# Performance work log

Hardware: AMD Instinct MI355X
Metric: run time of the kernel (lower is better)

Reference implementation:

```python
import jax, jax.numpy as jnp
import numpy as np

N_NODES = 100000
N_EDGES = 3200000
IN_CH = 256


def setup_inputs() -> dict:
    key = jax.random.key(0)
    k1, k2, k3 = jax.random.split(key, 3)
    x = jax.random.normal(k1, (N_NODES, IN_CH), dtype=jnp.float32)
    edge_index = jax.random.randint(k2, (2, N_EDGES), 0, N_NODES, dtype=jnp.int64)
    # GCNConv linear: weight [in_channels, 1] (applied as x @ W), bias [1]
    W = jax.random.normal(k3, (IN_CH, 1), dtype=jnp.float32) * (1.0 / np.sqrt(IN_CH))
    b = jnp.zeros((1,), dtype=jnp.float32)
    return {"x": x, "edge_index": edge_index, "W": W, "b": b}


def reference(x, edge_index, W, b):
    # PyG GCNConv(in, 1): h = x @ W; add self-loops; symmetric norm; scatter-add to target; + bias
    N = x.shape[0]
    self_loops = jnp.broadcast_to(jnp.arange(N, dtype=edge_index.dtype)[None, :], (2, N))
    ei = jnp.concatenate([edge_index, self_loops], axis=1)  # [2, E+N]
    src, dst = ei[0], ei[1]

    # degree computed at target (col) with unit edge weights, incl. self-loops
    deg = jax.ops.segment_sum(jnp.ones(ei.shape[1], dtype=x.dtype), dst, num_segments=N)
    deg_inv_sqrt = jnp.where(deg > 0, jax.lax.rsqrt(deg), 0.0)
    norm = deg_inv_sqrt[src] * deg_inv_sqrt[dst]  # [E+N]

    h = x @ W  # [N, 1] — project first (out_channels < in_channels)
    msg = norm[:, None] * h[src]  # [E+N, 1]
    out = jax.ops.segment_sum(msg, dst, num_segments=N)  # [N, 1]
    return out + b
```

## Files before the change

kernel.cpp:

```cpp
#include <hip/hip_runtime.h>

#define GCN_N 100000
#define GCN_E 3200000
#define GCN_C 256
#define BSHIFT 8
#define NBUCK 391
#define BCAP 9216

#define NBLK 512
#define TB 1024
#define CHUNK (GCN_E / NBLK)
#define EPT ((CHUNK + TB - 1) / TB)
#define ROWS ((GCN_N + NBLK - 1) / NBLK)

__global__ void k_init(int* __restrict__ cursor) {
    const int i = threadIdx.x;
    if (i < NBUCK) cursor[i] = 0;
}

__global__ void __launch_bounds__(TB) k_proj_bin(const float* __restrict__ x,
                                                 const float* __restrict__ W,
                                                 float* __restrict__ h,
                                                 const int* __restrict__ src,
                                                 const int* __restrict__ dst,
                                                 int* __restrict__ cursor,
                                                 int* __restrict__ bpack) {
    __shared__ int hist[NBUCK];
    __shared__ int lscan[NBUCK];
    __shared__ int gbase[NBUCK];
    __shared__ int wsum[16], woff[16];
    __shared__ int spack[CHUNK];
    __shared__ int sdest[CHUNK];
    const int tid = threadIdx.x, blk = blockIdx.x;
    const int lane = tid & 63, wv = tid >> 6;

    for (int b = tid; b < NBUCK; b += TB) hist[b] = 0;
    __syncthreads();

    const int c0 = blk * CHUNK;
    int my_pack[EPT], my_b[EPT], my_off[EPT];
    #pragma unroll
    for (int j = 0; j < EPT; ++j) {
        const int k = tid + j * TB;
        my_b[j] = -1;
        if (k < CHUNK) {
            const int d = dst[c0 + k];
            const int s = src[c0 + k];
            const int b = d >> BSHIFT;
            my_pack[j] = (s << BSHIFT) | (d & 255);
            my_b[j]    = b;
            my_off[j]  = atomicAdd(&hist[b], 1);
        }
    }

    {
        const float4 wf = *reinterpret_cast<const float4*>(W + lane * 4);
        const int r0 = blk * ROWS;
        const int r1 = min(r0 + ROWS, GCN_N);
        for (int i = r0 + wv; i < r1; i += 16) {
            const float4 xv = *reinterpret_cast<const float4*>(x + (size_t)i * GCN_C + lane * 4);
            float s = xv.x * wf.x + xv.y * wf.y + xv.z * wf.z + xv.w * wf.w;
            #pragma unroll
            for (int off = 32; off > 0; off >>= 1)
                s += __shfl_down(s, off, 64);
            if (lane == 0) h[i] = s;
        }
    }
    __syncthreads();

    if (tid < NBUCK) gbase[tid] = atomicAdd(&cursor[tid], hist[tid]);
    {
        const int v = (tid < NBUCK) ? hist[tid] : 0;
        int incl = v;
        #pragma unroll
        for (int d2 = 1; d2 < 64; d2 <<= 1) {
            const int t = __shfl_up(incl, d2, 64);
            if (lane >= d2) incl += t;
        }
        if (lane == 63) wsum[wv] = incl;
        __syncthreads();
        if (tid == 0) { int s = 0; for (int k2 = 0; k2 < 7; ++k2) { woff[k2] = s; s += wsum[k2]; } }
        __syncthreads();
        if (tid < NBUCK) lscan[tid] = incl - v + woff[wv];
    }
    __syncthreads();

    #pragma unroll
    for (int j = 0; j < EPT; ++j) {
        if (my_b[j] >= 0) {
            const int b    = my_b[j];
            const int slot = lscan[b] + my_off[j];
            const int goff = gbase[b] + my_off[j];
            spack[slot] = my_pack[j];
            sdest[slot] = (goff < BCAP) ? (b * BCAP + goff) : -1;
        }
    }
    __syncthreads();

    for (int i = tid; i < CHUNK; i += TB) {
        const int dpos = sdest[i];
        if (dpos >= 0) bpack[dpos] = spack[i];
    }
}

__global__ void __launch_bounds__(1024) k_deg_norm(const int* __restrict__ bpack,
                                                   const int* __restrict__ cursor,
                                                   const float* __restrict__ h,
                                                   float* __restrict__ dis,
                                                   float* __restrict__ g) {
    __shared__ int cnt[256];
    const int p = blockIdx.x, tid = threadIdx.x;
    if (tid < 256) cnt[tid] = 0;
    __syncthreads();
    const int s0 = p * BCAP, s1 = s0 + min(cursor[p], BCAP);
    for (int i = s0 + tid; i < s1; i += 1024)
        atomicAdd(&cnt[bpack[i] & 255], 1);
    __syncthreads();
    if (tid < 256) {
        const int node = (p << BSHIFT) + tid;
        if (node < GCN_N) {
            const float r = rsqrtf(1.0f + (float)cnt[tid]);
            dis[node] = r;
            g[node]   = r * h[node];
        }
    }
}

__global__ void __launch_bounds__(1024) k_scatter_bin(const int* __restrict__ bpack,
                                                      const int* __restrict__ cursor,
                                                      const float* __restrict__ g,
                                                      const float* __restrict__ dis,
                                                      const float* __restrict__ bias,
                                                      float* __restrict__ out) {
    __shared__ float acc[256];
    const int p = blockIdx.x, tid = threadIdx.x;
    if (tid < 256) acc[tid] = 0.0f;
    __syncthreads();
    const int s0 = p * BCAP, s1 = s0 + min(cursor[p], BCAP);
    for (int i = s0 + tid; i < s1; i += 1024) {
        const int pk = bpack[i];
        atomicAdd(&acc[pk & 255], g[pk >> BSHIFT]);
    }
    __syncthreads();
    if (tid < 256) {
        const int node = (p << BSHIFT) + tid;
        if (node < GCN_N)
            out[node] = bias[0] + dis[node] * (acc[tid] + g[node]);
    }
}

__global__ void k_zero(float* __restrict__ a, int n) {
    int i = blockIdx.x * blockDim.x + threadIdx.x;
    const int stride = gridDim.x * blockDim.x;
    for (; i < n; i += stride) a[i] = 0.0f;
}
__global__ void k_proj_sep(const float* __restrict__ x, const float* __restrict__ W,
                           float* __restrict__ h, int n) {
    const int lane   = threadIdx.x & 63;
    const int wave   = (blockIdx.x * blockDim.x + threadIdx.x) >> 6;
    const int nwaves = (gridDim.x * blockDim.x) >> 6;
    const float4 wf = *reinterpret_cast<const float4*>(W + lane * 4);
    for (int i = wave; i < n; i += nwaves) {
        const float4 xv = *reinterpret_cast<const float4*>(x + (size_t)i * GCN_C + lane * 4);
        float s = xv.x * wf.x + xv.y * wf.y + xv.z * wf.z + xv.w * wf.w;
        #pragma unroll
        for (int off = 32; off > 0; off >>= 1)
            s += __shfl_down(s, off, 64);
        if (lane == 0) h[i] = s;
    }
}
__global__ void k_degree_flat(const int* __restrict__ dst, float* __restrict__ deg, int e) {
    int i = blockIdx.x * blockDim.x + threadIdx.x;
    const int stride = gridDim.x * blockDim.x;
    for (; i < e; i += stride) atomicAdd(&deg[dst[i]], 1.0f);
}
__global__ void k_norm_flat(const float* __restrict__ h, float* __restrict__ deg_dis,
                            float* __restrict__ out, const float* __restrict__ bias, int n) {
    const int i = blockIdx.x * blockDim.x + threadIdx.x;
    if (i < n) {
        const float r = rsqrtf(deg_dis[i] + 1.0f);
        deg_dis[i] = r;
        out[i] = bias[0] + r * r * h[i];
    }
}
__global__ void k_scatter_flat(const int* __restrict__ src, const int* __restrict__ dst,
                               const float* __restrict__ h, const float* __restrict__ dis,
                               float* __restrict__ out, int e) {
    int i = blockIdx.x * blockDim.x + threadIdx.x;
    const int stride = gridDim.x * blockDim.x;
    for (; i < e; i += stride) {
        const int s = src[i], d = dst[i];
        atomicAdd(&out[d], dis[s] * dis[d] * h[s]);
    }
}

extern "C" void kernel_launch(void* const* d_in, const int* in_sizes, int n_in,
                              void* d_out, int out_size, void* d_ws, size_t ws_size,
                              hipStream_t stream) {
    const float* x  = (const float*)d_in[0];
    const int*   ei = (const int*)d_in[1];
    const float* W  = (const float*)d_in[2];
    const float* b  = (const float*)d_in[3];
    float* out = (float*)d_out;
    const int* src = ei;
    const int* dst = ei + GCN_E;

    float* h      = (float*)d_ws;
    float* dis    = h + GCN_N;
    float* g      = dis + GCN_N;
    int*   cursor = (int*)(g + GCN_N);
    int*   bpack  = cursor + NBUCK;
    const size_t need = ((size_t)3 * GCN_N + NBUCK + (size_t)NBUCK * BCAP) * 4;

    if (ws_size >= need) {
        k_init<<<1, 512, 0, stream>>>(cursor);
        k_proj_bin<<<NBLK, TB, 0, stream>>>(x, W, h, src, dst, cursor, bpack);
        k_deg_norm<<<NBUCK, 1024, 0, stream>>>(bpack, cursor, h, dis, g);
        k_scatter_bin<<<NBUCK, 1024, 0, stream>>>(bpack, cursor, g, dis, b, out);
    } else {
        float* hh  = (float*)d_ws;
        float* deg = hh + GCN_N;
        k_zero<<<512, 256, 0, stream>>>(deg, GCN_N);
        k_proj_sep<<<2048, 256, 0, stream>>>(x, W, hh, GCN_N);
        k_degree_flat<<<2048, 256, 0, stream>>>(dst, deg, GCN_E);
        k_norm_flat<<<(GCN_N + 255) / 256, 256, 0, stream>>>(hh, deg, out, b, GCN_N);
        k_scatter_flat<<<2048, 256, 0, stream>>>(src, dst, hh, deg, out, GCN_E);
    }
}
```

Before: 70.55 us.

## Split projection out of binning kernel and rebin with two-pass shared atomics

Moves the x@W projection from the fused binning kernel into its own grid-strided kernel launched before binning. The binning kernel no longer keeps per-thread edge arrays in registers. It counts a histogram in one pass, then rereads src/dst and claims slots with shared-memory atomic increments on the scanned offsets. This aims to lower register pressure and give both phases better occupancy. The cost is an extra kernel launch, reading the edge indices twice, and a nondeterministic order of edges within each bucket.

```diff
diff --git a/kernel.cpp b/kernel.cpp
--- a/kernel.cpp
+++ b/kernel.cpp
@@ -7,26 +7,38 @@
 #define NBUCK 391
 #define BCAP 9216
 
-#define NBLK 512
-#define TB 1024
-#define CHUNK (GCN_E / NBLK)
-#define EPT ((CHUNK + TB - 1) / TB)
-#define ROWS ((GCN_N + NBLK - 1) / NBLK)
+#define NBIN 512
+#define TBB 1024
+#define CHUNK (GCN_E / NBIN)
 
 __global__ void k_init(int* __restrict__ cursor) {
     const int i = threadIdx.x;
     if (i < NBUCK) cursor[i] = 0;
 }
 
-__global__ void __launch_bounds__(TB) k_proj_bin(const float* __restrict__ x,
-                                                 const float* __restrict__ W,
-                                                 float* __restrict__ h,
-                                                 const int* __restrict__ src,
-                                                 const int* __restrict__ dst,
-                                                 int* __restrict__ cursor,
-                                                 int* __restrict__ bpack) {
+__global__ void k_proj(const float* __restrict__ x, const float* __restrict__ W,
+                       float* __restrict__ h, int n) {
+    const int lane   = threadIdx.x & 63;
+    const int wave   = (blockIdx.x * blockDim.x + threadIdx.x) >> 6;
+    const int nwaves = (gridDim.x * blockDim.x) >> 6;
+    const float4 wf = *reinterpret_cast<const float4*>(W + lane * 4);
+    for (int i = wave; i < n; i += nwaves) {
+        const float4 xv = *reinterpret_cast<const float4*>(x + (size_t)i * GCN_C + lane * 4);
+        float s = xv.x * wf.x + xv.y * wf.y + xv.z * wf.z + xv.w * wf.w;
+        #pragma unroll
+        for (int off = 32; off > 0; off >>= 1)
+            s += __shfl_down(s, off, 64);
+        if (lane == 0) h[i] = s;
+    }
+}
+
+__global__ void __launch_bounds__(TBB) k_bin(const int* __restrict__ src,
+                                             const int* __restrict__ dst,
+                                             int* __restrict__ cursor,
+                                             int* __restrict__ bpack) {
     __shared__ int hist[NBUCK];
     __shared__ int lscan[NBUCK];
+    __shared__ int scan0[NBUCK];
     __shared__ int gbase[NBUCK];
     __shared__ int wsum[16], woff[16];
     __shared__ int spack[CHUNK];
@@ -34,38 +46,12 @@
     const int tid = threadIdx.x, blk = blockIdx.x;
     const int lane = tid & 63, wv = tid >> 6;
 
-    for (int b = tid; b < NBUCK; b += TB) hist[b] = 0;
+    for (int b = tid; b < NBUCK; b += TBB) hist[b] = 0;
     __syncthreads();
 
     const int c0 = blk * CHUNK;
-    int my_pack[EPT], my_b[EPT], my_off[EPT];
-    #pragma unroll
-    for (int j = 0; j < EPT; ++j) {
-        const int k = tid + j * TB;
-        my_b[j] = -1;
-        if (k < CHUNK) {
-            const int d = dst[c0 + k];
-            const int s = src[c0 + k];
-            const int b = d >> BSHIFT;
-            my_pack[j] = (s << BSHIFT) | (d & 255);
-            my_b[j]    = b;
-            my_off[j]  = atomicAdd(&hist[b], 1);
-        }
-    }
-
-    {
-        const float4 wf = *reinterpret_cast<const float4*>(W + lane * 4);
-        const int r0 = blk * ROWS;
-        const int r1 = min(r0 + ROWS, GCN_N);
-        for (int i = r0 + wv; i < r1; i += 16) {
-            const float4 xv = *reinterpret_cast<const float4*>(x + (size_t)i * GCN_C + lane * 4);
-            float s = xv.x * wf.x + xv.y * wf.y + xv.z * wf.z + xv.w * wf.w;
-            #pragma unroll
-            for (int off = 32; off > 0; off >>= 1)
-                s += __shfl_down(s, off, 64);
-            if (lane == 0) h[i] = s;
-        }
-    }
+    for (int k = tid; k < CHUNK; k += TBB)
+        atomicAdd(&hist[dst[c0 + k] >> BSHIFT], 1);
     __syncthreads();
 
     if (tid < NBUCK) gbase[tid] = atomicAdd(&cursor[tid], hist[tid]);
@@ -81,23 +67,26 @@
         __syncthreads();
         if (tid == 0) { int s = 0; for (int k2 = 0; k2 < 7; ++k2) { woff[k2] = s; s += wsum[k2]; } }
         __syncthreads();
-        if (tid < NBUCK) lscan[tid] = incl - v + woff[wv];
-    }
-    __syncthreads();
-
-    #pragma unroll
-    for (int j = 0; j < EPT; ++j) {
-        if (my_b[j] >= 0) {
-            const int b    = my_b[j];
-            const int slot = lscan[b] + my_off[j];
-            const int goff = gbase[b] + my_off[j];
-            spack[slot] = my_pack[j];
-            sdest[slot] = (goff < BCAP) ? (b * BCAP + goff) : -1;
+        if (tid < NBUCK) {
+            const int e = incl - v + woff[wv];
+            lscan[tid] = e;
+            scan0[tid] = e;
         }
     }
     __syncthreads();
 
-    for (int i = tid; i < CHUNK; i += TB) {
+    for (int k = tid; k < CHUNK; k += TBB) {
+        const int d = dst[c0 + k];
+        const int s = src[c0 + k];
+        const int b = d >> BSHIFT;
+        const int slot = atomicAdd(&lscan[b], 1);
+        const int goff = gbase[b] + (slot - scan0[b]);
+        spack[slot] = (s << BSHIFT) | (d & 255);
+        sdest[slot] = (goff < BCAP) ? (b * BCAP + goff) : -1;
+    }
+    __syncthreads();
+
+    for (int i = tid; i < CHUNK; i += TBB) {
         const int dpos = sdest[i];
         if (dpos >= 0) bpack[dpos] = spack[i];
     }
@@ -153,21 +142,6 @@
     int i = blockIdx.x * blockDim.x + threadIdx.x;
     const int stride = gridDim.x * blockDim.x;
     for (; i < n; i += stride) a[i] = 0.0f;
-}
-__global__ void k_proj_sep(const float* __restrict__ x, const float* __restrict__ W,
-                           float* __restrict__ h, int n) {
-    const int lane   = threadIdx.x & 63;
-    const int wave   = (blockIdx.x * blockDim.x + threadIdx.x) >> 6;
-    const int nwaves = (gridDim.x * blockDim.x) >> 6;
-    const float4 wf = *reinterpret_cast<const float4*>(W + lane * 4);
-    for (int i = wave; i < n; i += nwaves) {
-        const float4 xv = *reinterpret_cast<const float4*>(x + (size_t)i * GCN_C + lane * 4);
-        float s = xv.x * wf.x + xv.y * wf.y + xv.z * wf.z + xv.w * wf.w;
-        #pragma unroll
-        for (int off = 32; off > 0; off >>= 1)
-            s += __shfl_down(s, off, 64);
-        if (lane == 0) h[i] = s;
-    }
 }
 __global__ void k_degree_flat(const int* __restrict__ dst, float* __restrict__ deg, int e) {
     int i = blockIdx.x * blockDim.x + threadIdx.x;
@@ -214,14 +188,15 @@
 
     if (ws_size >= need) {
         k_init<<<1, 512, 0, stream>>>(cursor);
-        k_proj_bin<<<NBLK, TB, 0, stream>>>(x, W, h, src, dst, cursor, bpack);
+        k_proj<<<2048, 256, 0, stream>>>(x, W, h, GCN_N);
+        k_bin<<<NBIN, TBB, 0, stream>>>(src, dst, cursor, bpack);
         k_deg_norm<<<NBUCK, 1024, 0, stream>>>(bpack, cursor, h, dis, g);
         k_scatter_bin<<<NBUCK, 1024, 0, stream>>>(bpack, cursor, g, dis, b, out);
     } else {
         float* hh  = (float*)d_ws;
         float* deg = hh + GCN_N;
         k_zero<<<512, 256, 0, stream>>>(deg, GCN_N);
-        k_proj_sep<<<2048, 256, 0, stream>>>(x, W, hh, GCN_N);
+        k_proj<<<2048, 256, 0, stream>>>(x, W, hh, GCN_N);
         k_degree_flat<<<2048, 256, 0, stream>>>(dst, deg, GCN_E);
         k_norm_flat<<<(GCN_N + 255) / 256, 256, 0, stream>>>(hh, deg, out, b, GCN_N);
         k_scatter_flat<<<2048, 256, 0, stream>>>(src, dst, hh, deg, out, GCN_E);
```

After: 75.48 us. 7.0% more time.
